# Optimization experiments

Hardware: AMD Instinct MI355X
Metric: run time of the kernel (lower is better)

The kernel has to match this reference:

```python
import jax, jax.numpy as jnp
import numpy as np

N, E, G = 150000, 600000, 5000
NI, EI, GF, H, C = 16, 8, 32, 64, 40


def setup_inputs() -> dict:
    key = jax.random.key(0)
    ks = jax.random.split(key, 20)
    s = lambda fan: 1.0 / np.sqrt(fan)
    return {
        "x": jax.random.normal(ks[0], (N, NI), jnp.float32),
        "edge_index": jax.random.randint(ks[1], (2, E), 0, N),
        "edge_attr": jax.random.normal(ks[2], (E, EI), jnp.float32),
        "batch": jnp.sort(jax.random.randint(ks[3], (N,), 0, G)),
        "pocket_features": jax.random.normal(ks[4], (G, GF), jnp.float32),
        # edge MLP: Linear(EI,H) -> ReLU -> Linear(H, H*NI)
        "W_e1": jax.random.normal(ks[5], (EI, H), jnp.float32) * s(EI),
        "b_e1": jnp.zeros((H,), jnp.float32),
        "W_e2": jax.random.normal(ks[6], (H, H * NI), jnp.float32) * s(H),
        "b_e2": jnp.zeros((H * NI,), jnp.float32),
        # NNConv root weight + bias
        "root": jax.random.normal(ks[7], (NI, H), jnp.float32) * s(NI),
        "conv_bias": jnp.zeros((H,), jnp.float32),
        # GlobalAttention gate Linear(H,1)
        "Wg": jax.random.normal(ks[8], (H, 1), jnp.float32) * s(H),
        "bg": jnp.zeros((1,), jnp.float32),
        # fc1: input is concat [h_node(H), global_ctx(H), pocket(GF)]
        "W_fc1": jax.random.normal(ks[9], (2 * H + GF, H), jnp.float32) * s(2 * H + GF),
        "b_fc1": jnp.zeros((H,), jnp.float32),
        "W_np": jax.random.normal(ks[10], (H, C), jnp.float32) * s(H),
        "b_np": jnp.zeros((C,), jnp.float32),
        "W_sp": jax.random.normal(ks[11], (H, 1), jnp.float32) * s(H),
        "b_sp": jnp.zeros((1,), jnp.float32),
    }


def reference(x, edge_index, edge_attr, batch, pocket_features,
              W_e1, b_e1, W_e2, b_e2, root, conv_bias, Wg, bg,
              W_fc1, b_fc1, W_np, b_np, W_sp, b_sp):
    n, ni = x.shape
    h = root.shape[1]
    g = pocket_features.shape[0]
    src, dst = edge_index[0], edge_index[1]

    # NNConv: edge MLP -> per-edge weight matrix [E, NI, H]
    eh = jax.nn.relu(edge_attr @ W_e1 + b_e1)
    We = (eh @ W_e2 + b_e2).reshape(-1, ni, h)
    msg = jnp.einsum('ei,eih->eh', x[src], We)          # per-edge matmul
    agg = jax.ops.segment_sum(msg, dst, num_segments=n)
    cnt = jax.ops.segment_sum(jnp.ones(msg.shape[0], x.dtype), dst, num_segments=n)
    agg = agg / jnp.maximum(cnt, 1.0)[:, None]          # aggr='mean'
    h_node = jax.nn.relu(agg + x @ root + conv_bias)    # [N, H]

    # GlobalAttention pooling: scatter-softmax over nodes per graph
    gate = (h_node @ Wg + bg).squeeze(-1)               # [N]
    m = jax.ops.segment_max(gate, batch, num_segments=g)
    e = jnp.exp(gate - m[batch])
    denom = jax.ops.segment_sum(e, batch, num_segments=g)
    attn = e / denom[batch]
    gctx = jax.ops.segment_sum(attn[:, None] * h_node, batch, num_segments=g)
    gc = gctx[batch]                                    # broadcast back [N, H]

    feat = jnp.concatenate([h_node, gc, pocket_features[batch]], axis=1)
    f = jax.nn.relu(feat @ W_fc1 + b_fc1)
    node_pred = jax.nn.log_softmax(f @ W_np + b_np, axis=-1)
    stop = jax.nn.sigmoid((gc @ W_sp + b_sp).squeeze(-1))
    return node_pred, stop
```

## Files before the change

kernel.cpp:

```cpp
#include <hip/hip_runtime.h>
#include <hip/hip_bf16.h>
#include <math.h>

#define NN 150000
#define EE 600000
#define GG 5000
#define NI 16
#define EI 8
#define GFD 32
#define HH 64
#define CC 40

#define W2SZ (68 * 1024)
#define FPAD 68
#define NBLK ((NN + 1023) / 1024)

typedef __attribute__((ext_vector_type(8))) short short8v;
typedef __attribute__((ext_vector_type(16))) float f32x16;
typedef __attribute__((ext_vector_type(2))) float f32x2;

__device__ __forceinline__ unsigned short f2bf(float f) {
    __hip_bfloat16 h = __float2bfloat16(f);
    return __builtin_bit_cast(unsigned short, h);
}
__device__ __forceinline__ float bf2f(unsigned short u) {
    return __uint_as_float(((unsigned)u) << 16);
}
__device__ __forceinline__ unsigned cvtpk(float lo, float hi) {
    unsigned r;
    asm("v_cvt_pk_bf16_f32 %0, %1, %2" : "=v"(r) : "v"(lo), "v"(hi));
    return r;
}
__device__ __forceinline__ f32x2 pkmul(f32x2 a, f32x2 b) {
    f32x2 p;
    asm("v_pk_mul_f32 %0, %1, %2" : "=v"(p) : "v"(a), "v"(b));
    return p;
}
__device__ __forceinline__ short8v zfrag(float eh, const f32x2 (&xs2)[4]) {
    f32x2 ehp; ehp[0] = eh; ehp[1] = eh;
    union { short8v v; unsigned u[4]; } A;
    #pragma unroll
    for (int q = 0; q < 4; ++q) {
        f32x2 p = pkmul(ehp, xs2[q]);
        A.u[q] = cvtpk(p[0], p[1]);
    }
    return A.v;
}
__device__ __forceinline__ short8v xfrag(const f32x2 (&xs2)[4]) {
    union { short8v v; unsigned u[4]; } A;
    #pragma unroll
    for (int q = 0; q < 4; ++q)
        A.u[q] = cvtpk(xs2[q][0], xs2[q][1]);
    return A.v;
}

__global__ void k0_prep(const float* __restrict__ W_e2, const float* __restrict__ b_e2,
                        const float* __restrict__ W_fc1, const float* __restrict__ W_np,
                        const float* __restrict__ W_e1,
                        unsigned short* __restrict__ W2c,
                        unsigned short* __restrict__ W1aT,
                        unsigned short* __restrict__ W_npT,
                        unsigned short* __restrict__ W1e,
                        int* __restrict__ cursor)
{
    int idx = blockIdx.x * 256 + threadIdx.x;
    if (idx < W2SZ) {
        int c = idx >> 10, rem = idx & 1023;
        int r = rem >> 4, kk = rem & 15;
        float v = 0.f;
        if (c < 64)       v = W_e2[c * 1024 + kk * 64 + r];
        else if (c == 64) v = b_e2[kk * 64 + r];
        W2c[idx] = f2bf(v);
    } else if (idx < W2SZ + 4096) {
        int i = idx - W2SZ;
        int h = i >> 6, k = i & 63;
        W1aT[i] = f2bf(W_fc1[k * 64 + h]);
    } else if (idx < W2SZ + 8192) {
        int i = idx - W2SZ - 4096;
        int c = i >> 6, h = i & 63;
        W_npT[i] = f2bf(c < CC ? W_np[h * CC + c] : 0.f);
    } else if (idx < W2SZ + 8704) {
        int i = idx - W2SZ - 8192;
        int col = i >> 3, q = i & 7;
        W1e[i] = f2bf(W_e1[q * 64 + col]);
    } else if (idx < W2SZ + 8704 + NN) {
        cursor[idx - W2SZ - 8704] = 0;
    }
}

__global__ void kE_local(const int* __restrict__ ei, int* __restrict__ cursor,
                         int* __restrict__ rank)
{
    int e = blockIdx.x * 256 + threadIdx.x;
    if (e < EE) rank[e] = atomicAdd(&cursor[ei[EE + e]], 1);
}

__global__ void kB_scan1(const int* __restrict__ cnt, int* __restrict__ base,
                         int* __restrict__ bsum)
{
    __shared__ int sS[256];
    int b = blockIdx.x, t = threadIdx.x;
    int i0 = b * 1024 + t * 4;
    int v0 = (i0 + 0 < NN) ? cnt[i0 + 0] : 0;
    int v1 = (i0 + 1 < NN) ? cnt[i0 + 1] : 0;
    int v2 = (i0 + 2 < NN) ? cnt[i0 + 2] : 0;
    int v3 = (i0 + 3 < NN) ? cnt[i0 + 3] : 0;
    int tot = v0 + v1 + v2 + v3;
    sS[t] = tot;
    __syncthreads();
    int acc = tot;
    for (int off = 1; off < 256; off <<= 1) {
        int xv = (t >= off) ? sS[t - off] : 0;
        __syncthreads();
        acc += xv;
        sS[t] = acc;
        __syncthreads();
    }
    int run = acc - tot;
    if (i0 + 0 < NN) base[i0 + 0] = run; run += v0;
    if (i0 + 1 < NN) base[i0 + 1] = run; run += v1;
    if (i0 + 2 < NN) base[i0 + 2] = run; run += v2;
    if (i0 + 3 < NN) base[i0 + 3] = run;
    if (t == 255) bsum[b] = acc;
}

__global__ void kC_scan2(int* __restrict__ bsum)
{
    __shared__ int sS[256];
    int t = threadIdx.x;
    int v = (t < NBLK) ? bsum[t] : 0;
    sS[t] = v;
    __syncthreads();
    int acc = v;
    for (int off = 1; off < 256; off <<= 1) {
        int xv = (t >= off) ? sS[t - off] : 0;
        __syncthreads();
        acc += xv;
        sS[t] = acc;
        __syncthreads();
    }
    if (t < NBLK) bsum[t] = acc - v;
}

__device__ __forceinline__ void mfma_step(
    const unsigned short (&sEHT)[65][256], int c, int pf,
    const unsigned short* __restrict__ Bq0, const unsigned short* __restrict__ Bq1,
    int mb, int mr, const f32x2 (&xs0)[4], const f32x2 (&xs1)[4],
    short8v& curb0, short8v& curb1,
    f32x16& acc00, f32x16& acc01, f32x16& acc10, f32x16& acc11)
{
    short8v n0 = *(const short8v*)(Bq0 + pf * 1024);
    short8v n1 = *(const short8v*)(Bq1 + pf * 1024);
    int cc = (c & 31) << 1;
    float eh0 = bf2f(sEHT[c][(mb + mr) ^ cc]);
    float eh1 = bf2f(sEHT[c][(mb + 32 + mr) ^ cc]);
    short8v a0 = zfrag(eh0, xs0);
    short8v a1 = zfrag(eh1, xs1);
    __builtin_amdgcn_s_setprio(1);
    acc00 = __builtin_amdgcn_mfma_f32_32x32x16_bf16(a0, curb0, acc00, 0, 0, 0);
    acc01 = __builtin_amdgcn_mfma_f32_32x32x16_bf16(a0, curb1, acc01, 0, 0, 0);
    acc10 = __builtin_amdgcn_mfma_f32_32x32x16_bf16(a1, curb0, acc10, 0, 0, 0);
    acc11 = __builtin_amdgcn_mfma_f32_32x32x16_bf16(a1, curb1, acc11, 0, 0, 0);
    __builtin_amdgcn_s_setprio(0);
    curb0 = n0; curb1 = n1;
}

template<bool TWOPHASE>
__global__ __launch_bounds__(256, 4) void k1_mfma(
    const float* __restrict__ x, const int* __restrict__ ei,
    const float* __restrict__ ea,
    const unsigned short* __restrict__ W1e, const float* __restrict__ b_e1,
    const unsigned short* __restrict__ W2c,
    const int* __restrict__ rank, const int* __restrict__ base,
    const int* __restrict__ bsum,
    unsigned* __restrict__ msg16, float* __restrict__ agg)
{
    __shared__ unsigned short sEHT[65][256];
    __shared__ int sIdx[256];

    const int t = threadIdx.x;
    const long long eb = (long long)blockIdx.x * 256;

    const int lane = t & 63;
    const int w = t >> 6;
    const int mr = lane & 31;
    const int half = lane >> 5;
    const int mb = w * 64;

    {
        long long ge = eb + t;
        if (ge < EE) {
            int d = ei[EE + ge];
            sIdx[t] = TWOPHASE ? (base[d] + bsum[d >> 10] + rank[ge]) : d;
        } else {
            sIdx[t] = -1;
        }
        sEHT[64][t] = (unsigned short)0x3F80;
    }

    {
        short8v bW0, bW1;
        if (half == 0) {
            bW0 = *(const short8v*)(W1e + (size_t)mr * 8);
            bW1 = *(const short8v*)(W1e + (size_t)(32 + mr) * 8);
        } else {
            #pragma unroll
            for (int q = 0; q < 8; ++q) { bW0[q] = 0; bW1[q] = 0; }
        }
        float bias0 = b_e1[mr];
        float bias1 = b_e1[32 + mr];
        #pragma unroll
        for (int m = 0; m < 2; ++m) {
            int e_loc = w * 64 + m * 32 + mr;
            long long ge = eb + e_loc;
            short8v a;
            if (half == 0 && ge < EE) {
                const float4* eap = (const float4*)(ea + ge * EI);
                float4 u0 = eap[0], u1 = eap[1];
                union { short8v v; unsigned u[4]; } A;
                A.u[0] = cvtpk(u0.x, u0.y); A.u[1] = cvtpk(u0.z, u0.w);
                A.u[2] = cvtpk(u1.x, u1.y); A.u[3] = cvtpk(u1.z, u1.w);
                a = A.v;
            } else {
                #pragma unroll
                for (int q = 0; q < 8; ++q) a[q] = 0;
            }
            #pragma unroll
            for (int n = 0; n < 2; ++n) {
                f32x16 c_;
                #pragma unroll
                for (int r = 0; r < 16; ++r) c_[r] = 0.f;
                c_ = __builtin_amdgcn_mfma_f32_32x32x16_bf16(a, n ? bW1 : bW0, c_, 0, 0, 0);
                int kcol = n * 32 + mr;
                float bias = n ? bias1 : bias0;
                #pragma unroll
                for (int r = 0; r < 16; r += 2) {
                    int row = (r & 3) + 8 * (r >> 2) + 4 * half;
                    int e0 = w * 64 + m * 32 + row;
                    float v0 = fmaxf(c_[r]     + bias, 0.f);
                    float v1 = fmaxf(c_[r + 1] + bias, 0.f);
                    *(unsigned*)&sEHT[kcol][e0 ^ (mr << 1)] = cvtpk(v0, v1);
                }
            }
        }
    }

    f32x2 xs0[4], xs1[4];
    {
        long long e0 = eb + mb + mr;
        long long e1 = eb + mb + 32 + mr;
        if (e0 < EE) {
            int s0 = ei[e0];
            const float4* xp = (const float4*)(x + (size_t)s0 * NI + half * 8);
            float4 u0 = xp[0], u1 = xp[1];
            xs0[0][0]=u0.x; xs0[0][1]=u0.y; xs0[1][0]=u0.z; xs0[1][1]=u0.w;
            xs0[2][0]=u1.x; xs0[2][1]=u1.y; xs0[3][0]=u1.z; xs0[3][1]=u1.w;
        } else {
            #pragma unroll
            for (int q = 0; q < 4; ++q) { xs0[q][0] = 0.f; xs0[q][1] = 0.f; }
        }
        if (e1 < EE) {
            int s1 = ei[e1];
            const float4* xp = (const float4*)(x + (size_t)s1 * NI + half * 8);
            float4 u0 = xp[0], u1 = xp[1];
            xs1[0][0]=u0.x; xs1[0][1]=u0.y; xs1[1][0]=u0.z; xs1[1][1]=u0.w;
            xs1[2][0]=u1.x; xs1[2][1]=u1.y; xs1[3][0]=u1.z; xs1[3][1]=u1.w;
        } else {
            #pragma unroll
            for (int q = 0; q < 4; ++q) { xs1[q][0] = 0.f; xs1[q][1] = 0.f; }
        }
    }
    __syncthreads();

    f32x16 acc00, acc01, acc10, acc11;
    #pragma unroll
    for (int r = 0; r < 16; ++r) { acc00[r] = 0.f; acc01[r] = 0.f; acc10[r] = 0.f; acc11[r] = 0.f; }

    const unsigned short* Bq0 = W2c + mr * 16 + half * 8;
    const unsigned short* Bq1 = Bq0 + 512;

    short8v bA0 = *(const short8v*)(Bq0);
    short8v bA1 = *(const short8v*)(Bq1);
    short8v bB0 = *(const short8v*)(Bq0 + 1024);
    short8v bB1 = *(const short8v*)(Bq1 + 1024);

    #pragma unroll 2
    for (int c = 0; c < 64; c += 2) {
        mfma_step(sEHT, c,     c + 2, Bq0, Bq1, mb, mr, xs0, xs1, bA0, bA1, acc00, acc01, acc10, acc11);
        mfma_step(sEHT, c + 1, c + 3, Bq0, Bq1, mb, mr, xs0, xs1, bB0, bB1, acc00, acc01, acc10, acc11);
    }
    {
        short8v a0 = xfrag(xs0);
        short8v a1 = xfrag(xs1);
        __builtin_amdgcn_s_setprio(1);
        acc00 = __builtin_amdgcn_mfma_f32_32x32x16_bf16(a0, bA0, acc00, 0, 0, 0);
        acc01 = __builtin_amdgcn_mfma_f32_32x32x16_bf16(a0, bA1, acc01, 0, 0, 0);
        acc10 = __builtin_amdgcn_mfma_f32_32x32x16_bf16(a1, bA0, acc10, 0, 0, 0);
        acc11 = __builtin_amdgcn_mfma_f32_32x32x16_bf16(a1, bA1, acc11, 0, 0, 0);
        __builtin_amdgcn_s_setprio(0);
    }

    #pragma unroll
    for (int r = 0; r < 16; ++r) {
        int row = (r & 3) + 8 * (r >> 2) + 4 * half;
        int i0 = sIdx[mb + row];
        int i1 = sIdx[mb + 32 + row];
        if (TWOPHASE) {
            if (i0 >= 0) msg16[(size_t)i0 * 32 + mr] = cvtpk(acc00[r], acc01[r]);
            if (i1 >= 0) msg16[(size_t)i1 * 32 + mr] = cvtpk(acc10[r], acc11[r]);
        } else {
            if (i0 >= 0) {
                atomicAdd(&agg[(size_t)i0 * 64 + mr],      acc00[r]);
                atomicAdd(&agg[(size_t)i0 * 64 + 32 + mr], acc01[r]);
            }
            if (i1 >= 0) {
                atomicAdd(&agg[(size_t)i1 * 64 + mr],      acc10[r]);
                atomicAdd(&agg[(size_t)i1 * 64 + 32 + mr], acc11[r]);
            }
        }
    }
}

__global__ __launch_bounds__(256) void k2_red(
    const unsigned* __restrict__ msg16, const int* __restrict__ base,
    const int* __restrict__ bsum,
    const float* __restrict__ x, const float* __restrict__ root,
    const float* __restrict__ conv_bias,
    unsigned short* __restrict__ hn16,
    const float* __restrict__ Wg, const float* __restrict__ bg,
    float* __restrict__ gate)
{
    __shared__ float sroot[16][64];
    int t = threadIdx.x;
    #pragma unroll
    for (int q = 0; q < 4; ++q) {
        int i = q * 256 + t;
        sroot[i >> 6][i & 63] = root[i];
    }
    __syncthreads();

    int n = blockIdx.x * 4 + (t >> 6);
    int l = t & 63;
    int mr = l & 31, so = l >> 5;
    int s = base[n] + bsum[n >> 10];
    int e = (n == NN - 1) ? EE : base[n + 1] + bsum[(n + 1) >> 10];

    float alo = 0.f, ahi = 0.f;
    for (int sl = s + so; sl < e; sl += 2) {
        unsigned u = msg16[(size_t)sl * 32 + mr];
        alo += __uint_as_float(u << 16);
        ahi += __uint_as_float(u & 0xFFFF0000u);
    }
    alo += __shfl_xor(alo, 32);
    ahi += __shfl_xor(ahi, 32);
    float acc = (l < 32) ? alo : ahi;

    float inv = 1.0f / fmaxf((float)(e - s), 1.0f);
    float v = acc * inv + conv_bias[l];
    float xv = (l < 16) ? x[(size_t)n * NI + l] : 0.f;
    #pragma unroll
    for (int i = 0; i < 16; ++i)
        v = fmaf(__shfl(xv, i), sroot[i][l], v);
    v = fmaxf(v, 0.f);
    hn16[(size_t)n * 64 + l] = f2bf(v);

    float gv = v * Wg[l];
    #pragma unroll
    for (int off = 32; off; off >>= 1) gv += __shfl_xor(gv, off);
    if (l == 0) gate[n] = gv + bg[0];
}

__global__ __launch_bounds__(256) void k2_node(
    const float* __restrict__ agg, const int* __restrict__ base,
    const int* __restrict__ bsum,
    const float* __restrict__ x, const float* __restrict__ root,
    const float* __restrict__ conv_bias,
    unsigned short* __restrict__ hn16,
    const float* __restrict__ Wg, const float* __restrict__ bg,
    float* __restrict__ gate)
{
    int t = threadIdx.x;
    int n = blockIdx.x * 4 + (t >> 6);
    int h = t & 63;
    int s = base[n] + bsum[n >> 10];
    int e = (n == NN - 1) ? EE : base[n + 1] + bsum[(n + 1) >> 10];
    float inv = 1.0f / fmaxf((float)(e - s), 1.0f);
    float v = agg[(size_t)n * 64 + h] * inv + conv_bias[h];
    const float* xp = x + (size_t)n * NI;
    #pragma unroll
    for (int i = 0; i < NI; ++i) v += xp[i] * root[i * 64 + h];
    v = fmaxf(v, 0.f);
    hn16[(size_t)n * 64 + h] = f2bf(v);
    float gv = v * Wg[h];
    #pragma unroll
    for (int off = 32; off; off >>= 1) gv += __shfl_xor(gv, off);
    if (h == 0) gate[n] = gv + bg[0];
}

__device__ __forceinline__ int lbound(const int* __restrict__ b, int v) {
    int lo = 0, hi = NN;
    while (lo < hi) { int mid = (lo + hi) >> 1; if (b[mid] < v) lo = mid + 1; else hi = mid; }
    return lo;
}

__global__ __launch_bounds__(64) void k3_pool(
    const float* __restrict__ gate, const int* __restrict__ batch,
    const unsigned short* __restrict__ hn16, const float* __restrict__ pocket,
    const float* __restrict__ W_fc1, const float* __restrict__ b_fc1,
    const float* __restrict__ W_sp, const float* __restrict__ b_sp,
    float* __restrict__ pg, float* __restrict__ sg)
{
    int g = blockIdx.x;
    int lane = threadIdx.x;
    int s = lbound(batch, g);
    int e = lbound(batch, g + 1);

    float gcv = 0.f;
    if (e > s) {
        float m = -INFINITY;
        for (int n = s + lane; n < e; n += 64) m = fmaxf(m, gate[n]);
        #pragma unroll
        for (int off = 32; off; off >>= 1) m = fmaxf(m, __shfl_xor(m, off));
        float acc = 0.f, den = 0.f;
        for (int n = s; n < e; ++n) {
            float ev = expf(gate[n] - m);
            den += ev;
            acc += ev * bf2f(hn16[(size_t)n * 64 + lane]);
        }
        gcv = acc / den;
    }

    float sv = gcv * W_sp[lane];
    #pragma unroll
    for (int off = 32; off; off >>= 1) sv += __shfl_xor(sv, off);
    if (lane == 0) sg[g] = 1.f / (1.f + expf(-(sv + b_sp[0])));

    float pk = (lane < GFD) ? pocket[(size_t)g * GFD + lane] : 0.f;
    float pgv = b_fc1[lane];
    #pragma unroll 8
    for (int kk = 0; kk < 64; ++kk)
        pgv = fmaf(__shfl(gcv, kk), W_fc1[(64 + kk) * 64 + lane], pgv);
    #pragma unroll 8
    for (int kk = 0; kk < 32; ++kk)
        pgv = fmaf(__shfl(pk, kk), W_fc1[(128 + kk) * 64 + lane], pgv);
    pg[(size_t)g * 64 + lane] = pgv;
}

__global__ __launch_bounds__(256, 4) void k4_mfma(
    const unsigned short* __restrict__ hn16, const int* __restrict__ batch,
    const float* __restrict__ pg, const float* __restrict__ sg,
    const unsigned short* __restrict__ W1aT, const unsigned short* __restrict__ W_npT,
    const float* __restrict__ b_np,
    float* __restrict__ out_np, float* __restrict__ out_stop)
{
    __shared__ __align__(16) float sF[4][32][FPAD];
    __shared__ int sB[128];

    const int t = threadIdx.x;
    const int wv = t >> 6, lane = t & 63;
    const int mr = lane & 31, half = lane >> 5;
    const int nb = blockIdx.x * 128;

    if (t < 128) {
        int n = nb + t;
        sB[t] = (n < NN) ? batch[n] : 0;
    }

    const int node = nb + wv * 32 + mr;

    f32x16 acc0, acc1;
    #pragma unroll
    for (int r = 0; r < 16; ++r) { acc0[r] = 0.f; acc1[r] = 0.f; }

    #pragma unroll
    for (int c = 0; c < 4; ++c) {
        short8v a;
        if (node < NN) {
            a = *(const short8v*)(hn16 + (size_t)node * 64 + c * 16 + half * 8);
        } else {
            #pragma unroll
            for (int q = 0; q < 8; ++q) a[q] = 0;
        }
        short8v b0 = *(const short8v*)(W1aT + (size_t)mr * 64        + c * 16 + half * 8);
        short8v b1 = *(const short8v*)(W1aT + (size_t)(mr + 32) * 64 + c * 16 + half * 8);
        acc0 = __builtin_amdgcn_mfma_f32_32x32x16_bf16(a, b0, acc0, 0, 0, 0);
        acc1 = __builtin_amdgcn_mfma_f32_32x32x16_bf16(a, b1, acc1, 0, 0, 0);
    }
    __syncthreads();

    #pragma unroll
    for (int r = 0; r < 16; ++r) {
        int row = (r & 3) + 8 * (r >> 2) + 4 * half;
        int g = sB[wv * 32 + row];
        float p0 = pg[(size_t)g * 64 + mr];
        float p1 = pg[(size_t)g * 64 + 32 + mr];
        sF[wv][row][mr]      = fmaxf(acc0[r] + p0, 0.f);
        sF[wv][row][32 + mr] = fmaxf(acc1[r] + p1, 0.f);
    }

    f32x16 acc2, acc3;
    #pragma unroll
    for (int r = 0; r < 16; ++r) { acc2[r] = 0.f; acc3[r] = 0.f; }

    #pragma unroll
    for (int c = 0; c < 4; ++c) {
        const float* fp = &sF[wv][mr][c * 16 + half * 8];
        float4 u0 = *(const float4*)(fp);
        float4 u1 = *(const float4*)(fp + 4);
        union { short8v v; unsigned u[4]; } A;
        A.u[0] = cvtpk(u0.x, u0.y); A.u[1] = cvtpk(u0.z, u0.w);
        A.u[2] = cvtpk(u1.x, u1.y); A.u[3] = cvtpk(u1.z, u1.w);
        short8v a = A.v;
        short8v b0 = *(const short8v*)(W_npT + (size_t)mr * 64        + c * 16 + half * 8);
        short8v b1 = *(const short8v*)(W_npT + (size_t)(mr + 32) * 64 + c * 16 + half * 8);
        acc2 = __builtin_amdgcn_mfma_f32_32x32x16_bf16(a, b0, acc2, 0, 0, 0);
        acc3 = __builtin_amdgcn_mfma_f32_32x32x16_bf16(a, b1, acc3, 0, 0, 0);
    }

    float bn1 = b_np[mr];
    float bn2 = (mr < 8) ? b_np[32 + mr] : 0.f;

    #pragma unroll
    for (int r = 0; r < 16; ++r) {
        int row = (r & 3) + 8 * (r >> 2) + 4 * half;
        int n = nb + wv * 32 + row;
        float v1 = acc2[r] + bn1;
        float v2 = acc3[r] + bn2;
        float m = (mr < 8) ? fmaxf(v1, v2) : v1;
        #pragma unroll
        for (int off = 16; off; off >>= 1) m = fmaxf(m, __shfl_xor(m, off));
        float s = expf(v1 - m) + ((mr < 8) ? expf(v2 - m) : 0.f);
        #pragma unroll
        for (int off = 16; off; off >>= 1) s += __shfl_xor(s, off);
        float ls = m + logf(s);
        if (n < NN) {
            out_np[(size_t)n * CC + mr] = v1 - ls;
            if (mr < 8) out_np[(size_t)n * CC + 32 + mr] = v2 - ls;
            if (mr == 0) out_stop[n] = sg[sB[wv * 32 + row]];
        }
    }
}

extern "C" void kernel_launch(void* const* d_in, const int* in_sizes, int n_in,
                              void* d_out, int out_size, void* d_ws, size_t ws_size,
                              hipStream_t stream)
{
    (void)in_sizes; (void)n_in; (void)out_size;
    const float* x        = (const float*)d_in[0];
    const int*   ei       = (const int*)d_in[1];
    const float* ea       = (const float*)d_in[2];
    const int*   batch    = (const int*)d_in[3];
    const float* pocket   = (const float*)d_in[4];
    const float* W_e1     = (const float*)d_in[5];
    const float* b_e1     = (const float*)d_in[6];
    const float* W_e2     = (const float*)d_in[7];
    const float* b_e2     = (const float*)d_in[8];
    const float* root     = (const float*)d_in[9];
    const float* conv_b   = (const float*)d_in[10];
    const float* Wg       = (const float*)d_in[11];
    const float* bg       = (const float*)d_in[12];
    const float* W_fc1    = (const float*)d_in[13];
    const float* b_fc1    = (const float*)d_in[14];
    const float* W_np     = (const float*)d_in[15];
    const float* b_np     = (const float*)d_in[16];
    const float* W_sp     = (const float*)d_in[17];
    const float* b_sp     = (const float*)d_in[18];

    char* wsb = (char*)d_ws;
    float* agg    = (float*)wsb;
    int*   base   = (int*)(agg + (size_t)NN * 64);
    int*   bsum   = base + NN + 4;
    int*   cursor = bsum + 256;
    int*   rank   = cursor + NN;
    float* gate   = (float*)(rank + EE);
    float* pg     = gate + NN;
    float* sg     = pg + (size_t)GG * 64;
    unsigned short* hn16  = (unsigned short*)(sg + GG);
    unsigned short* W2c   = hn16 + (size_t)NN * 64;
    unsigned short* W1aT  = W2c + W2SZ;
    unsigned short* W_npT = W1aT + 4096;
    unsigned short* W1e   = W_npT + 4096;
    size_t head = (size_t)((char*)(W1e + 512) - wsb);
    size_t msg_off = (head + 255) & ~(size_t)255;
    unsigned* msg16 = (unsigned*)(wsb + msg_off);
    size_t need = msg_off + (size_t)EE * 32 * sizeof(unsigned);
    const bool twophase = (ws_size >= need);

    k0_prep<<<(W2SZ + 8704 + NN + 255) / 256, 256, 0, stream>>>(
        W_e2, b_e2, W_fc1, W_np, W_e1, W2c, W1aT, W_npT, W1e, cursor);

    kE_local<<<(EE + 255) / 256, 256, 0, stream>>>(ei, cursor, rank);
    kB_scan1<<<NBLK, 256, 0, stream>>>(cursor, base, bsum);
    kC_scan2<<<1, 256, 0, stream>>>(bsum);

    if (twophase) {
        k1_mfma<true><<<(EE + 255) / 256, 256, 0, stream>>>(
            x, ei, ea, W1e, b_e1, W2c, rank, base, bsum, msg16, agg);
        k2_red<<<NN / 4, 256, 0, stream>>>(msg16, base, bsum, x, root, conv_b,
                                           hn16, Wg, bg, gate);
    } else {
        hipMemsetAsync(agg, 0, (size_t)NN * 64 * sizeof(float), stream);
        k1_mfma<false><<<(EE + 255) / 256, 256, 0, stream>>>(
            x, ei, ea, W1e, b_e1, W2c, rank, base, bsum, msg16, agg);
        k2_node<<<NN / 4, 256, 0, stream>>>(agg, base, bsum, x, root, conv_b,
                                            hn16, Wg, bg, gate);
    }

    k3_pool<<<GG, 64, 0, stream>>>(gate, batch, hn16, pocket, W_fc1, b_fc1, W_sp, b_sp, pg, sg);

    float* out_np   = (float*)d_out;
    float* out_stop = out_np + (size_t)NN * CC;
    k4_mfma<<<(NN + 127) / 128, 256, 0, stream>>>(hn16, batch, pg, sg, W1aT, W_npT, b_np,
                                                  out_np, out_stop);
}
```

Baseline: 259.9 us.

## Replace two-pass scan with atomic block offsets, restructure edge-hidden LDS layout

The two-level prefix scan becomes a single kernel in which each block takes its offset through an atomicAdd on a global cursor, and the per-node degree is read from the cursor array. The message buffer is therefore grouped by destination in an arbitrary block order rather than in node order. The edge-hidden LDS tile moves from a transposed, XOR-swizzled layout to a row-major padded layout, so each lane reads eight bf16 values with one vector load per 8 MFMA steps instead of one scalar load per step. The reduction loops in k2_red and the pooling kernel are unrolled by two. This saves a kernel launch and some LDS traffic, at the cost of scalar 16-bit LDS stores that may cause bank conflicts.

```diff
diff --git a/kernel.cpp b/kernel.cpp
--- a/kernel.cpp
+++ b/kernel.cpp
@@ -12,10 +12,12 @@
 #define CC 40
 
 #define W2SZ (68 * 1024)
+#define EHS 72
 #define FPAD 68
 #define NBLK ((NN + 1023) / 1024)
 
 typedef __attribute__((ext_vector_type(8))) short short8v;
+typedef __attribute__((ext_vector_type(8))) unsigned short ushort8v;
 typedef __attribute__((ext_vector_type(16))) float f32x16;
 typedef __attribute__((ext_vector_type(2))) float f32x2;
 
@@ -61,7 +63,7 @@
                         unsigned short* __restrict__ W1aT,
                         unsigned short* __restrict__ W_npT,
                         unsigned short* __restrict__ W1e,
-                        int* __restrict__ cursor)
+                        int* __restrict__ cursor, int* __restrict__ gcur)
 {
     int idx = blockIdx.x * 256 + threadIdx.x;
     if (idx < W2SZ) {
@@ -85,6 +87,8 @@
         W1e[i] = f2bf(W_e1[q * 64 + col]);
     } else if (idx < W2SZ + 8704 + NN) {
         cursor[idx - W2SZ - 8704] = 0;
+    } else if (idx == W2SZ + 8704 + NN) {
+        gcur[0] = 0;
     }
 }
 
@@ -95,10 +99,11 @@
     if (e < EE) rank[e] = atomicAdd(&cursor[ei[EE + e]], 1);
 }
 
-__global__ void kB_scan1(const int* __restrict__ cnt, int* __restrict__ base,
-                         int* __restrict__ bsum)
+__global__ void kB_scan(const int* __restrict__ cnt, int* __restrict__ base,
+                        int* __restrict__ gcur)
 {
     __shared__ int sS[256];
+    __shared__ int sOff;
     int b = blockIdx.x, t = threadIdx.x;
     int i0 = b * 1024 + t * 4;
     int v0 = (i0 + 0 < NN) ? cnt[i0 + 0] : 0;
@@ -116,53 +121,13 @@
         sS[t] = acc;
         __syncthreads();
     }
-    int run = acc - tot;
+    if (t == 255) sOff = atomicAdd(gcur, acc);
+    __syncthreads();
+    int run = acc - tot + sOff;
     if (i0 + 0 < NN) base[i0 + 0] = run; run += v0;
     if (i0 + 1 < NN) base[i0 + 1] = run; run += v1;
     if (i0 + 2 < NN) base[i0 + 2] = run; run += v2;
     if (i0 + 3 < NN) base[i0 + 3] = run;
-    if (t == 255) bsum[b] = acc;
-}
-
-__global__ void kC_scan2(int* __restrict__ bsum)
-{
-    __shared__ int sS[256];
-    int t = threadIdx.x;
-    int v = (t < NBLK) ? bsum[t] : 0;
-    sS[t] = v;
-    __syncthreads();
-    int acc = v;
-    for (int off = 1; off < 256; off <<= 1) {
-        int xv = (t >= off) ? sS[t - off] : 0;
-        __syncthreads();
-        acc += xv;
-        sS[t] = acc;
-        __syncthreads();
-    }
-    if (t < NBLK) bsum[t] = acc - v;
-}
-
-__device__ __forceinline__ void mfma_step(
-    const unsigned short (&sEHT)[65][256], int c, int pf,
-    const unsigned short* __restrict__ Bq0, const unsigned short* __restrict__ Bq1,
-    int mb, int mr, const f32x2 (&xs0)[4], const f32x2 (&xs1)[4],
-    short8v& curb0, short8v& curb1,
-    f32x16& acc00, f32x16& acc01, f32x16& acc10, f32x16& acc11)
-{
-    short8v n0 = *(const short8v*)(Bq0 + pf * 1024);
-    short8v n1 = *(const short8v*)(Bq1 + pf * 1024);
-    int cc = (c & 31) << 1;
-    float eh0 = bf2f(sEHT[c][(mb + mr) ^ cc]);
-    float eh1 = bf2f(sEHT[c][(mb + 32 + mr) ^ cc]);
-    short8v a0 = zfrag(eh0, xs0);
-    short8v a1 = zfrag(eh1, xs1);
-    __builtin_amdgcn_s_setprio(1);
-    acc00 = __builtin_amdgcn_mfma_f32_32x32x16_bf16(a0, curb0, acc00, 0, 0, 0);
-    acc01 = __builtin_amdgcn_mfma_f32_32x32x16_bf16(a0, curb1, acc01, 0, 0, 0);
-    acc10 = __builtin_amdgcn_mfma_f32_32x32x16_bf16(a1, curb0, acc10, 0, 0, 0);
-    acc11 = __builtin_amdgcn_mfma_f32_32x32x16_bf16(a1, curb1, acc11, 0, 0, 0);
-    __builtin_amdgcn_s_setprio(0);
-    curb0 = n0; curb1 = n1;
 }
 
 template<bool TWOPHASE>
@@ -172,10 +137,9 @@
     const unsigned short* __restrict__ W1e, const float* __restrict__ b_e1,
     const unsigned short* __restrict__ W2c,
     const int* __restrict__ rank, const int* __restrict__ base,
-    const int* __restrict__ bsum,
     unsigned* __restrict__ msg16, float* __restrict__ agg)
 {
-    __shared__ unsigned short sEHT[65][256];
+    __shared__ unsigned short sEHT2[256][EHS];
     __shared__ int sIdx[256];
 
     const int t = threadIdx.x;
@@ -191,11 +155,10 @@
         long long ge = eb + t;
         if (ge < EE) {
             int d = ei[EE + ge];
-            sIdx[t] = TWOPHASE ? (base[d] + bsum[d >> 10] + rank[ge]) : d;
+            sIdx[t] = TWOPHASE ? (base[d] + rank[ge]) : d;
         } else {
             sIdx[t] = -1;
         }
-        sEHT[64][t] = (unsigned short)0x3F80;
     }
 
     {
@@ -211,8 +174,7 @@
         float bias1 = b_e1[32 + mr];
         #pragma unroll
         for (int m = 0; m < 2; ++m) {
-            int e_loc = w * 64 + m * 32 + mr;
-            long long ge = eb + e_loc;
+            long long ge = eb + mb + m * 32 + mr;
             short8v a;
             if (half == 0 && ge < EE) {
                 const float4* eap = (const float4*)(ea + ge * EI);
@@ -234,12 +196,9 @@
                 int kcol = n * 32 + mr;
                 float bias = n ? bias1 : bias0;
                 #pragma unroll
-                for (int r = 0; r < 16; r += 2) {
+                for (int r = 0; r < 16; ++r) {
                     int row = (r & 3) + 8 * (r >> 2) + 4 * half;
-                    int e0 = w * 64 + m * 32 + row;
-                    float v0 = fmaxf(c_[r]     + bias, 0.f);
-                    float v1 = fmaxf(c_[r + 1] + bias, 0.f);
-                    *(unsigned*)&sEHT[kcol][e0 ^ (mr << 1)] = cvtpk(v0, v1);
+                    sEHT2[mb + m * 32 + row][kcol] = f2bf(fmaxf(c_[r] + bias, 0.f));
                 }
             }
         }
@@ -247,10 +206,10 @@
 
     f32x2 xs0[4], xs1[4];
     {
-        long long e0 = eb + mb + mr;
-        long long e1 = eb + mb + 32 + mr;
-        if (e0 < EE) {
-            int s0 = ei[e0];
+        long long g0 = eb + mb + mr;
+        long long g1 = g0 + 32;
+        if (g0 < EE) {
+            int s0 = ei[g0];
             const float4* xp = (const float4*)(x + (size_t)s0 * NI + half * 8);
             float4 u0 = xp[0], u1 = xp[1];
             xs0[0][0]=u0.x; xs0[0][1]=u0.y; xs0[1][0]=u0.z; xs0[1][1]=u0.w;
@@ -259,8 +218,8 @@
             #pragma unroll
             for (int q = 0; q < 4; ++q) { xs0[q][0] = 0.f; xs0[q][1] = 0.f; }
         }
-        if (e1 < EE) {
-            int s1 = ei[e1];
+        if (g1 < EE) {
+            int s1 = ei[g1];
             const float4* xp = (const float4*)(x + (size_t)s1 * NI + half * 8);
             float4 u0 = xp[0], u1 = xp[1];
             xs1[0][0]=u0.x; xs1[0][1]=u0.y; xs1[1][0]=u0.z; xs1[1][1]=u0.w;
@@ -284,10 +243,47 @@
     short8v bB0 = *(const short8v*)(Bq0 + 1024);
     short8v bB1 = *(const short8v*)(Bq1 + 1024);
 
-    #pragma unroll 2
-    for (int c = 0; c < 64; c += 2) {
-        mfma_step(sEHT, c,     c + 2, Bq0, Bq1, mb, mr, xs0, xs1, bA0, bA1, acc00, acc01, acc10, acc11);
-        mfma_step(sEHT, c + 1, c + 3, Bq0, Bq1, mb, mr, xs0, xs1, bB0, bB1, acc00, acc01, acc10, acc11);
+    const unsigned short* ehp0 = &sEHT2[mb + mr][0];
+    const unsigned short* ehp1 = ehp0 + 32 * EHS;
+
+    ushort8v eh0 = *(const ushort8v*)(ehp0);
+    ushort8v eh1 = *(const ushort8v*)(ehp1);
+
+    #pragma unroll 1
+    for (int cb = 0; cb < 64; cb += 8) {
+        ushort8v nx0 = *(const ushort8v*)(ehp0 + cb + 8);
+        ushort8v nx1 = *(const ushort8v*)(ehp1 + cb + 8);
+        #pragma unroll
+        for (int j = 0; j < 8; j += 2) {
+            int c = cb + j;
+            {
+                short8v p0 = *(const short8v*)(Bq0 + (c + 2) * 1024);
+                short8v p1 = *(const short8v*)(Bq1 + (c + 2) * 1024);
+                short8v a0 = zfrag(bf2f(eh0[j]), xs0);
+                short8v a1 = zfrag(bf2f(eh1[j]), xs1);
+                __builtin_amdgcn_s_setprio(1);
+                acc00 = __builtin_amdgcn_mfma_f32_32x32x16_bf16(a0, bA0, acc00, 0, 0, 0);
+                acc01 = __builtin_amdgcn_mfma_f32_32x32x16_bf16(a0, bA1, acc01, 0, 0, 0);
+                acc10 = __builtin_amdgcn_mfma_f32_32x32x16_bf16(a1, bA0, acc10, 0, 0, 0);
+                acc11 = __builtin_amdgcn_mfma_f32_32x32x16_bf16(a1, bA1, acc11, 0, 0, 0);
+                __builtin_amdgcn_s_setprio(0);
+                bA0 = p0; bA1 = p1;
+            }
+            {
+                short8v p0 = *(const short8v*)(Bq0 + (c + 3) * 1024);
+                short8v p1 = *(const short8v*)(Bq1 + (c + 3) * 1024);
+                short8v a0 = zfrag(bf2f(eh0[j + 1]), xs0);
+                short8v a1 = zfrag(bf2f(eh1[j + 1]), xs1);
+                __builtin_amdgcn_s_setprio(1);
+                acc00 = __builtin_amdgcn_mfma_f32_32x32x16_bf16(a0, bB0, acc00, 0, 0, 0);
+                acc01 = __builtin_amdgcn_mfma_f32_32x32x16_bf16(a0, bB1, acc01, 0, 0, 0);
+                acc10 = __builtin_amdgcn_mfma_f32_32x32x16_bf16(a1, bB0, acc10, 0, 0, 0);
+                acc11 = __builtin_amdgcn_mfma_f32_32x32x16_bf16(a1, bB1, acc11, 0, 0, 0);
+                __builtin_amdgcn_s_setprio(0);
+                bB0 = p0; bB1 = p1;
+            }
+        }
+        eh0 = nx0; eh1 = nx1;
     }
     {
         short8v a0 = xfrag(xs0);
@@ -323,7 +319,7 @@
 
 __global__ __launch_bounds__(256) void k2_red(
     const unsigned* __restrict__ msg16, const int* __restrict__ base,
-    const int* __restrict__ bsum,
+    const int* __restrict__ deg,
     const float* __restrict__ x, const float* __restrict__ root,
     const float* __restrict__ conv_bias,
     unsigned short* __restrict__ hn16,
@@ -342,11 +338,18 @@
     int n = blockIdx.x * 4 + (t >> 6);
     int l = t & 63;
     int mr = l & 31, so = l >> 5;
-    int s = base[n] + bsum[n >> 10];
-    int e = (n == NN - 1) ? EE : base[n + 1] + bsum[(n + 1) >> 10];
+    int s = base[n];
+    int e = s + deg[n];
 
     float alo = 0.f, ahi = 0.f;
-    for (int sl = s + so; sl < e; sl += 2) {
+    int sl = s + so;
+    for (; sl + 2 < e; sl += 4) {
+        unsigned u0 = msg16[(size_t)sl * 32 + mr];
+        unsigned u1 = msg16[(size_t)(sl + 2) * 32 + mr];
+        alo += __uint_as_float(u0 << 16) + __uint_as_float(u1 << 16);
+        ahi += __uint_as_float(u0 & 0xFFFF0000u) + __uint_as_float(u1 & 0xFFFF0000u);
+    }
+    if (sl < e) {
         unsigned u = msg16[(size_t)sl * 32 + mr];
         alo += __uint_as_float(u << 16);
         ahi += __uint_as_float(u & 0xFFFF0000u);
@@ -371,8 +374,7 @@
 }
 
 __global__ __launch_bounds__(256) void k2_node(
-    const float* __restrict__ agg, const int* __restrict__ base,
-    const int* __restrict__ bsum,
+    const float* __restrict__ agg, const int* __restrict__ deg,
     const float* __restrict__ x, const float* __restrict__ root,
     const float* __restrict__ conv_bias,
     unsigned short* __restrict__ hn16,
@@ -382,9 +384,7 @@
     int t = threadIdx.x;
     int n = blockIdx.x * 4 + (t >> 6);
     int h = t & 63;
-    int s = base[n] + bsum[n >> 10];
-    int e = (n == NN - 1) ? EE : base[n + 1] + bsum[(n + 1) >> 10];
-    float inv = 1.0f / fmaxf((float)(e - s), 1.0f);
+    float inv = 1.0f / fmaxf((float)deg[n], 1.0f);
     float v = agg[(size_t)n * 64 + h] * inv + conv_bias[h];
     const float* xp = x + (size_t)n * NI;
     #pragma unroll
@@ -422,10 +422,20 @@
         #pragma unroll
         for (int off = 32; off; off >>= 1) m = fmaxf(m, __shfl_xor(m, off));
         float acc = 0.f, den = 0.f;
-        for (int n = s; n < e; ++n) {
+        int n = s;
+        for (; n + 2 <= e; n += 2) {
+            float e0 = expf(gate[n] - m);
+            float e1 = expf(gate[n + 1] - m);
+            float h0 = bf2f(hn16[(size_t)n * 64 + lane]);
+            float h1 = bf2f(hn16[(size_t)(n + 1) * 64 + lane]);
+            den += e0 + e1;
+            acc = fmaf(e0, h0, acc);
+            acc = fmaf(e1, h1, acc);
+        }
+        if (n < e) {
             float ev = expf(gate[n] - m);
             den += ev;
-            acc += ev * bf2f(hn16[(size_t)n * 64 + lane]);
+            acc = fmaf(ev, bf2f(hn16[(size_t)n * 64 + lane]), acc);
         }
         gcv = acc / den;
     }
@@ -569,8 +579,8 @@
     char* wsb = (char*)d_ws;
     float* agg    = (float*)wsb;
     int*   base   = (int*)(agg + (size_t)NN * 64);
-    int*   bsum   = base + NN + 4;
-    int*   cursor = bsum + 256;
+    int*   gcur   = base + NN;
+    int*   cursor = gcur + 4;
     int*   rank   = cursor + NN;
     float* gate   = (float*)(rank + EE);
     float* pg     = gate + NN;
@@ -586,23 +596,22 @@
     size_t need = msg_off + (size_t)EE * 32 * sizeof(unsigned);
     const bool twophase = (ws_size >= need);
 
-    k0_prep<<<(W2SZ + 8704 + NN + 255) / 256, 256, 0, stream>>>(
-        W_e2, b_e2, W_fc1, W_np, W_e1, W2c, W1aT, W_npT, W1e, cursor);
+    k0_prep<<<(W2SZ + 8705 + NN + 255) / 256, 256, 0, stream>>>(
+        W_e2, b_e2, W_fc1, W_np, W_e1, W2c, W1aT, W_npT, W1e, cursor, gcur);
 
     kE_local<<<(EE + 255) / 256, 256, 0, stream>>>(ei, cursor, rank);
-    kB_scan1<<<NBLK, 256, 0, stream>>>(cursor, base, bsum);
-    kC_scan2<<<1, 256, 0, stream>>>(bsum);
+    kB_scan<<<NBLK, 256, 0, stream>>>(cursor, base, gcur);
 
     if (twophase) {
         k1_mfma<true><<<(EE + 255) / 256, 256, 0, stream>>>(
-            x, ei, ea, W1e, b_e1, W2c, rank, base, bsum, msg16, agg);
-        k2_red<<<NN / 4, 256, 0, stream>>>(msg16, base, bsum, x, root, conv_b,
+            x, ei, ea, W1e, b_e1, W2c, rank, base, msg16, agg);
+        k2_red<<<NN / 4, 256, 0, stream>>>(msg16, base, cursor, x, root, conv_b,
                                            hn16, Wg, bg, gate);
     } else {
         hipMemsetAsync(agg, 0, (size_t)NN * 64 * sizeof(float), stream);
         k1_mfma<false><<<(EE + 255) / 256, 256, 0, stream>>>(
-            x, ei, ea, W1e, b_e1, W2c, rank, base, bsum, msg16, agg);
-        k2_node<<<NN / 4, 256, 0, stream>>>(agg, base, bsum, x, root, conv_b,
+            x, ei, ea, W1e, b_e1, W2c, rank, base, msg16, agg);
+        k2_node<<<NN / 4, 256, 0, stream>>>(agg, cursor, x, root, conv_b,
                                             hn16, Wg, bg, gate);
     }
 
```

New measurement: 262.0 us. Within noise of the previous version (+0.8%).
